# Optimization experiments

Hardware: AMD Instinct MI355X
Metric: run time of the kernel (lower is better)

## Reference

```python
import jax, jax.numpy as jnp
import numpy as np

B, Q, P, HID, H, KV, D = 2, 1024, 3072, 4096, 32, 8, 128
G = H // KV          # GQA group size
EPS = 1e-6
ROPE_THETA = 1e6


def setup_inputs() -> dict:
    key = jax.random.key(0)
    ks = jax.random.split(key, 8)
    hidden_states = jax.random.normal(ks[0], (B, Q, HID), jnp.float32)
    # real RoPE tables for positions [P, P+Q) (extend phase)
    pos = jnp.arange(P, P + Q, dtype=jnp.float32)
    inv_freq = 1.0 / (ROPE_THETA ** (jnp.arange(0, D, 2, dtype=jnp.float32) / D))
    freqs = pos[:, None] * inv_freq[None, :]            # [Q, D/2]
    emb = jnp.concatenate([freqs, freqs], axis=-1)       # [Q, D]
    cos = jnp.broadcast_to(jnp.cos(emb)[None], (B, Q, D)).astype(jnp.float32)
    sin = jnp.broadcast_to(jnp.sin(emb)[None], (B, Q, D)).astype(jnp.float32)
    k_cache = jax.random.normal(ks[1], (B, KV, P, D), jnp.float32)
    v_cache = jax.random.normal(ks[2], (B, KV, P, D), jnp.float32)
    s = 0.02
    Wq = jax.random.normal(ks[3], (HID, H * D), jnp.float32) * s
    Wk = jax.random.normal(ks[4], (HID, KV * D), jnp.float32) * s
    Wv = jax.random.normal(ks[5], (HID, KV * D), jnp.float32) * s
    Wo = jax.random.normal(ks[6], (H * D, HID), jnp.float32) * s
    q_norm_w = jnp.ones((D,), jnp.float32)
    k_norm_w = jnp.ones((D,), jnp.float32)
    return dict(hidden_states=hidden_states, cos=cos, sin=sin,
                k_cache=k_cache, v_cache=v_cache,
                Wq=Wq, Wk=Wk, Wv=Wv, Wo=Wo,
                q_norm_w=q_norm_w, k_norm_w=k_norm_w)


def _rmsnorm(x, w):
    var = jnp.mean(x * x, axis=-1, keepdims=True)
    return x * jax.lax.rsqrt(var + EPS) * w


def _rotate_half(x):
    x1, x2 = jnp.split(x, 2, axis=-1)
    return jnp.concatenate([-x2, x1], axis=-1)


def _rope(x, cos, sin):
    # x: [B, h, Q, D]; cos/sin: [B, Q, D] -> broadcast over heads
    c = cos[:, None, :, :]
    s = sin[:, None, :, :]
    return x * c + _rotate_half(x) * s


def reference(hidden_states, cos, sin, k_cache, v_cache,
              Wq, Wk, Wv, Wo, q_norm_w, k_norm_w):
    # projections
    q = (hidden_states @ Wq).reshape(B, Q, H, D)
    k = (hidden_states @ Wk).reshape(B, Q, KV, D)
    v = (hidden_states @ Wv).reshape(B, Q, KV, D)
    # per-head RMSNorm on q and k
    q = _rmsnorm(q, q_norm_w)
    k = _rmsnorm(k, k_norm_w)
    # [B, heads, Q, D]
    q = q.transpose(0, 2, 1, 3)
    k = k.transpose(0, 2, 1, 3)
    v = v.transpose(0, 2, 1, 3)
    q = _rope(q, cos, sin)
    k = _rope(k, cos, sin)
    # extend: concat cached prefix KV with new KV -> kv_len = P + Q
    K = jnp.concatenate([k_cache, k], axis=2)   # [B, KV, P+Q, D]
    V = jnp.concatenate([v_cache, v], axis=2)
    qg = q.reshape(B, KV, G, Q, D)
    scale = 1.0 / jnp.sqrt(jnp.float32(D))
    scores = jnp.einsum('bkgqd,bksd->bkgqs', qg, K) * scale  # [B,KV,G,Q,P+Q]
    # causal mask offset by prefix: query i sees keys <= P + i
    key_idx = jnp.arange(P + Q)
    mask = key_idx[None, :] <= (P + jnp.arange(Q))[:, None]  # [Q, P+Q]
    scores = jnp.where(mask[None, None, None], scores, jnp.float32(-1e30))
    attn = jax.nn.softmax(scores, axis=-1)
    out = jnp.einsum('bkgqs,bksd->bkgqd', attn, V)           # [B,KV,G,Q,D]
    out = out.reshape(B, H, Q, D).transpose(0, 2, 1, 3).reshape(B, Q, H * D)
    return out @ Wo
```

## Files before the change

kernel.cpp:

```cpp
#include <hip/hip_runtime.h>
#include <hip/hip_bf16.h>

#define B_ 2
#define Q_ 1024
#define P_ 3072
#define HID_ 4096
#define H_ 32
#define KV_ 8
#define D_ 128
#define S_ 4096
#define NQKV 6144
#define QSCALE 0.1275174432f

typedef __attribute__((ext_vector_type(4))) float f32x4;
typedef __attribute__((ext_vector_type(8))) unsigned short u16x8;
typedef __attribute__((ext_vector_type(4))) unsigned short u16x4;
typedef __attribute__((ext_vector_type(8))) __bf16 bf16x8;

__device__ __forceinline__ unsigned short f2bf(float f){
  unsigned u = __builtin_bit_cast(unsigned, f);
  unsigned r = (u + 0x7FFFu + ((u >> 16) & 1u)) >> 16;
  return (unsigned short)r;
}
__device__ __forceinline__ unsigned pk2bf(float lo, float hi){
  unsigned r;
  asm("v_cvt_pk_bf16_f32 %0, %1, %2" : "=v"(r) : "v"(lo), "v"(hi));
  return r;
}
__device__ __forceinline__ f32x4 mfma16(u16x8 a, u16x8 b, f32x4 c){
  return __builtin_amdgcn_mfma_f32_16x16x32_bf16(
      __builtin_bit_cast(bf16x8, a), __builtin_bit_cast(bf16x8, b), c, 0, 0, 0);
}
typedef const __attribute__((address_space(1))) void* gp1_t;
typedef __attribute__((address_space(3))) void* lp3_t;
__device__ __forceinline__ void gl16(const unsigned short* g, unsigned short* l){
  __builtin_amdgcn_global_load_lds((gp1_t)g, (lp3_t)l, 16, 0, 0);
}

#define N1_ 2097152
#define N2_ 1572864
__global__ __launch_bounds__(256) void prep(
    const float* __restrict__ hs, const float* __restrict__ kc,
    unsigned short* __restrict__ AH, unsigned short* __restrict__ Kb){
  const int PD = P_ * D_;
  const long SD = (long)S_ * D_;
  for(int i4 = blockIdx.x * 256 + threadIdx.x; i4 < N1_ + N2_; i4 += gridDim.x * 256){
    if(i4 < N1_){
      long i = (long)i4 * 4;
      float4 x = *(const float4*)(hs + i);
      *(u16x4*)(AH + i) = (u16x4){f2bf(x.x), f2bf(x.y), f2bf(x.z), f2bf(x.w)};
    } else {
      long i = (long)(i4 - N1_) * 4;
      int bkv = (int)(i / PD);
      int rem = (int)(i - (long)bkv * PD);
      long dst = (long)bkv * SD + rem;
      float4 k4 = *(const float4*)(kc + i);
      *(u16x4*)(Kb + dst) = (u16x4){f2bf(k4.x), f2bf(k4.y), f2bf(k4.z), f2bf(k4.w)};
    }
  }
}

__global__ __launch_bounds__(256) void convert_w(
    const float* __restrict__ Wq, const float* __restrict__ Wk,
    const float* __restrict__ Wv, const float* __restrict__ Wo,
    unsigned short* __restrict__ WT, unsigned short* __restrict__ WoT){
  __shared__ float tile[64][65];
  int x = blockIdx.x;
  const float* W; int ldn, n_off; unsigned short* dst; int n0;
  if(x < 64)      { W = Wq; ldn = 4096; n_off = 0;    dst = WT;  n0 = x * 64; }
  else if(x < 80) { W = Wk; ldn = 1024; n_off = 4096; dst = WT;  n0 = (x-64) * 64; }
  else if(x < 96) { W = Wv; ldn = 1024; n_off = 5120; dst = WT;  n0 = (x-80) * 64; }
  else            { W = Wo; ldn = 4096; n_off = 0;    dst = WoT; n0 = (x-96) * 64; }
  int k0 = blockIdx.y * 64;
  int tid = threadIdx.x;
  int r = tid >> 4, c = (tid & 15) * 4;
  #pragma unroll
  for(int j = 0; j < 4; ++j){
    float4 v = *(const float4*)(W + (long)(k0 + r + j*16) * ldn + n0 + c);
    tile[r + j*16][c] = v.x; tile[r + j*16][c+1] = v.y;
    tile[r + j*16][c+2] = v.z; tile[r + j*16][c+3] = v.w;
  }
  __syncthreads();
  #pragma unroll
  for(int j = 0; j < 4; ++j){
    int n = r + j*16;
    long o = (long)(n_off + n0 + n) * 4096 + k0 + c;
    *(u16x4*)(dst + o) = (u16x4){f2bf(tile[c][n]), f2bf(tile[c+1][n]),
                                 f2bf(tile[c+2][n]), f2bf(tile[c+3][n])};
  }
}

__global__ __launch_bounds__(256) void cache_vt(
    const float* __restrict__ vc, unsigned short* __restrict__ VT){
  __shared__ unsigned short T[128][72];
  int bkv = blockIdx.y;
  int s0 = blockIdx.x * 64;
  int tid = threadIdx.x;
  int r = tid >> 2, dblk = (tid & 3) * 32;
  const float* src = vc + ((long)bkv * P_ + s0 + r) * 128 + dblk;
  #pragma unroll
  for(int u = 0; u < 8; ++u){
    float4 v = *(const float4*)(src + u*4);
    T[dblk + u*4 + 0][r] = f2bf(v.x);
    T[dblk + u*4 + 1][r] = f2bf(v.y);
    T[dblk + u*4 + 2][r] = f2bf(v.z);
    T[dblk + u*4 + 3][r] = f2bf(v.w);
  }
  __syncthreads();
  int d = tid >> 1, sh = (tid & 1) * 32;
  unsigned short* dst = VT + ((long)bkv * 128 + d) * S_ + s0 + sh;
  #pragma unroll
  for(int u = 0; u < 4; ++u){
    u16x8 v;
    #pragma unroll
    for(int j = 0; j < 8; ++j) v[j] = T[d][sh + u*8 + j];
    *(u16x8*)(dst + u*8) = v;
  }
}

__global__ __launch_bounds__(128) void maxw(
    const float* __restrict__ qw, const float* __restrict__ kw, float* __restrict__ M){
  __shared__ float sa[2], sb[2];
  int t = threadIdx.x;
  float a = fabsf(qw[t]), b = fabsf(kw[t]);
  #pragma unroll
  for(int o = 32; o; o >>= 1){
    a = fmaxf(a, __shfl_xor(a, o));
    b = fmaxf(b, __shfl_xor(b, o));
  }
  if((t & 63) == 0){ sa[t >> 6] = a; sb[t >> 6] = b; }
  __syncthreads();
  if(t == 0){
    float mq = fmaxf(sa[0], sa[1]), mk = fmaxf(sb[0], sb[1]);
    M[0] = 128.0f * QSCALE * mq * mk * 1.01f + 0.25f;
  }
}

__global__ __launch_bounds__(256) void gemm_bf16(
    const unsigned short* __restrict__ Ag, const unsigned short* __restrict__ Bg,
    float* __restrict__ C, int nbx, int ldc){
  __shared__ __align__(16) unsigned short sA[4096], sB[4096];
  int tid = threadIdx.x;
  int nwg = nbx * 16;
  int lin = blockIdx.x;
  int cpx = nwg >> 3;
  int swz = (lin & 7) * cpx + (lin >> 3);
  int by = swz & 15, bx = swz >> 4;
  int m0 = by * 128, n0 = bx * 128;
  int lane = tid & 63, w = tid >> 6;
  int lr = lane & 15, lg = lane >> 4;
  int wm = (w >> 1) * 64, wn = (w & 1) * 64;
  int rowi = w * 16 + (lane >> 2);
  int cchunk = ((lane & 3) ^ ((lane >> 3) & 3)) << 3;
  const unsigned short* aP = Ag + (long)(m0 + rowi) * 4096 + cchunk;
  const unsigned short* bP = Bg + (long)(n0 + rowi) * 4096 + cchunk;
  const int step2 = 64 * 4096;
  unsigned short* dA = sA + w * 512;
  unsigned short* dB = sB + w * 512;
  int rdcol = (lg * 8) ^ (((lr >> 1) & 3) << 3);
  f32x4 zero = {0.f,0.f,0.f,0.f};
  f32x4 acc[4][4];
  #pragma unroll
  for(int mi=0;mi<4;++mi)
    #pragma unroll
    for(int ni=0;ni<4;++ni) acc[mi][ni] = zero;

  for(int kt = 0; kt < 128; ++kt){
    int kk = kt * 32;
    __syncthreads();
    gl16(aP + kk, dA);  gl16(aP + step2 + kk, dA + 2048);
    gl16(bP + kk, dB);  gl16(bP + step2 + kk, dB + 2048);
    __syncthreads();
    u16x8 ah[4];
    #pragma unroll
    for(int mi = 0; mi < 4; ++mi)
      ah[mi] = *(const u16x8*)(sA + (wm + mi*16 + lr) * 32 + rdcol);
    #pragma unroll
    for(int ni = 0; ni < 4; ++ni){
      u16x8 bh = *(const u16x8*)(sB + (wn + ni*16 + lr) * 32 + rdcol);
      #pragma unroll
      for(int mi = 0; mi < 4; ++mi)
        acc[mi][ni] = mfma16(ah[mi], bh, acc[mi][ni]);
    }
  }
  #pragma unroll
  for(int mi = 0; mi < 4; ++mi)
    #pragma unroll
    for(int r = 0; r < 4; ++r){
      long rowoff = (long)(m0 + wm + mi*16 + lg*4 + r) * ldc + n0 + wn + lr;
      #pragma unroll
      for(int ni = 0; ni < 4; ++ni)
        C[rowoff + ni*16] = acc[mi][ni][r];
    }
}

__global__ __launch_bounds__(256) void pp_qkv(
    const float* __restrict__ Craw, const float* __restrict__ cosb,
    const float* __restrict__ sinb, const float* __restrict__ qw,
    const float* __restrict__ kw, unsigned short* __restrict__ Qb,
    unsigned short* __restrict__ Kb, unsigned short* __restrict__ VT){
  int rid = blockIdx.x * 4 + (threadIdx.x >> 6);
  int lane = threadIdx.x & 63;
  if(rid < 65536){
    int b = rid >> 15;
    int rem = rid & 32767;
    int q = rem >> 5;
    int h = rem & 31;
    long rowoff = (long)(b * Q_ + q) * NQKV + h * 128;
    float x1 = Craw[rowoff + lane];
    float x2 = Craw[rowoff + 64 + lane];
    float ss = x1*x1 + x2*x2;
    for(int o = 32; o; o >>= 1) ss += __shfl_xor(ss, o);
    float norm = rsqrtf(ss * (1.0f/128.0f) + 1e-6f);
    float xn1 = x1 * norm * qw[lane];
    float xn2 = x2 * norm * qw[64 + lane];
    long co = (long)(b * Q_ + q) * 128;
    float c1 = cosb[co + lane],      s1 = sinb[co + lane];
    float c2 = cosb[co + 64 + lane], s2 = sinb[co + 64 + lane];
    float o1 = (xn1 * c1 - xn2 * s1) * QSCALE;
    float o2 = (xn2 * c2 + xn1 * s2) * QSCALE;
    long dst = ((long)(b * H_ + h) * Q_ + q) * 128;
    Qb[dst + lane] = f2bf(o1);
    Qb[dst + 64 + lane] = f2bf(o2);
  } else {
    int rid2 = rid - 65536;
    int b = rid2 >> 13;
    int rem = rid2 & 8191;
    int q = rem >> 3;
    int kv = rem & 7;
    int bkv = b * KV_ + kv;
    long rowoff = (long)(b * Q_ + q) * NQKV;
    float x1 = Craw[rowoff + 4096 + kv*128 + lane];
    float x2 = Craw[rowoff + 4096 + kv*128 + 64 + lane];
    float ss = x1*x1 + x2*x2;
    for(int o = 32; o; o >>= 1) ss += __shfl_xor(ss, o);
    float norm = rsqrtf(ss * (1.0f/128.0f) + 1e-6f);
    float xn1 = x1 * norm * kw[lane];
    float xn2 = x2 * norm * kw[64 + lane];
    long co = (long)(b * Q_ + q) * 128;
    float c1 = cosb[co + lane],      s1 = sinb[co + lane];
    float c2 = cosb[co + 64 + lane], s2 = sinb[co + 64 + lane];
    long dst = ((long)bkv * S_ + P_ + q) * 128;
    Kb[dst + lane]      = f2bf(xn1 * c1 - xn2 * s1);
    Kb[dst + 64 + lane] = f2bf(xn2 * c2 + xn1 * s2);
    float v1 = Craw[rowoff + 5120 + kv*128 + lane];
    float v2 = Craw[rowoff + 5120 + kv*128 + 64 + lane];
    VT[((long)bkv * 128 + lane) * S_ + P_ + q]      = f2bf(v1);
    VT[((long)bkv * 128 + 64 + lane) * S_ + P_ + q] = f2bf(v2);
  }
}

#define KVB 32
#define PSL 40
__global__ __launch_bounds__(256, 2) void attn(
    const unsigned short* __restrict__ Qg, const unsigned short* __restrict__ Kg,
    const unsigned short* __restrict__ VTg, const float* __restrict__ Mp,
    float* __restrict__ po, float* __restrict__ pl){
  __shared__ __align__(16) unsigned short Ks[2][KVB*128];
  __shared__ __align__(16) unsigned short Vs[2][128*KVB];
  __shared__ __align__(16) unsigned short Ps[4][64*PSL];
  int tid = threadIdx.x;
  int qb = blockIdx.x >> 1, sp = blockIdx.x & 1;
  int b = blockIdx.z, h = blockIdx.y, q0 = qb * 256;
  int kvh = h >> 2;
  int w = tid >> 6, lane = tid & 63, lr = lane & 15, lg = lane >> 4;
  int q0w = q0 + w * 64;
  float Mv = Mp[0];
  u16x8 qh[4][4];
  #pragma unroll
  for(int mi = 0; mi < 4; ++mi){
    long qbase = ((long)(b * H_ + h) * Q_ + q0w + mi*16 + lr) * 128;
    #pragma unroll
    for(int c = 0; c < 4; ++c)
      qh[mi][c] = *(const u16x8*)(Qg + qbase + c*32 + lg*8);
  }
  f32x4 minit = {-Mv, -Mv, -Mv, -Mv};
  f32x4 zero = {0.f,0.f,0.f,0.f};
  f32x4 o[4][8];
  #pragma unroll
  for(int mi = 0; mi < 4; ++mi)
    #pragma unroll
    for(int i = 0; i < 8; ++i) o[mi][i] = zero;
  float l[4] = {0.f, 0.f, 0.f, 0.f};
  long kb  = (long)(b * KV_ + kvh) * S_ * 128;
  long vb0 = (long)(b * KV_ + kvh) * 128 * (long)S_;
  int T = 104 + 8 * qb;
  int half = T >> 1;
  int t0 = sp ? half : 0;
  int t1 = sp ? T : half;
  int koff[2], voff[2], ldst[2];
  #pragma unroll
  for(int i = 0; i < 2; ++i){
    int L = (w*2 + i)*64 + lane;
    ldst[i] = L * 8;
    int r = L >> 4, c8 = (L & 15) ^ (r & 7);
    koff[i] = r*128 + c8*8;
    int d = L >> 2, sc = (L & 3) ^ (d & 3) ^ ((d >> 2) & 3);
    voff[i] = d*S_ + sc*8;
  }
  {
    const unsigned short* kg = Kg + kb + (long)t0 * (KVB*128);
    const unsigned short* vg = VTg + vb0 + t0 * KVB;
    #pragma unroll
    for(int i = 0; i < 2; ++i){
      gl16(kg + koff[i], &Ks[t0 & 1][ldst[i]]);
      gl16(vg + voff[i], &Vs[t0 & 1][ldst[i]]);
    }
  }
  __syncthreads();

  int lr7 = lr & 7;
  for(int t = t0; t < t1; ++t){
    int cur = t & 1;
    if(t + 1 < t1){
      int s1 = (t + 1) * KVB;
      const unsigned short* kg = Kg + kb + (long)s1 * 128;
      const unsigned short* vg = VTg + vb0 + s1;
      #pragma unroll
      for(int i = 0; i < 2; ++i){
        gl16(kg + koff[i], &Ks[cur^1][ldst[i]]);
        gl16(vg + voff[i], &Vs[cur^1][ldst[i]]);
      }
    }
    int s0 = t * KVB;
    if(s0 <= P_ + q0w + 63){
      f32x4 pacc[4][2];
      #pragma unroll
      for(int mi = 0; mi < 4; ++mi){ pacc[mi][0] = minit; pacc[mi][1] = minit; }
      __builtin_amdgcn_s_setprio(1);
      #pragma unroll
      for(int c = 0; c < 4; ++c)
        #pragma unroll
        for(int ni = 0; ni < 2; ++ni){
          u16x8 kh = *(const u16x8*)(&Ks[cur][(ni*16 + lr)*128 + (((c*4 + lg) ^ lr7) << 3)]);
          #pragma unroll
          for(int mi = 0; mi < 4; ++mi)
            pacc[mi][ni] = mfma16(kh, qh[mi][c], pacc[mi][ni]);
        }
      __builtin_amdgcn_s_setprio(0);
      if(s0 + KVB - 1 > P_ + q0w){
        #pragma unroll
        for(int mi = 0; mi < 4; ++mi){
          int qrow = q0w + mi*16 + lr;
          #pragma unroll
          for(int ni = 0; ni < 2; ++ni)
            #pragma unroll
            for(int r = 0; r < 4; ++r){
              int skey = s0 + ni*16 + lg*4 + r;
              if(skey > P_ + qrow) pacc[mi][ni][r] = -1e30f;
            }
        }
      }
      #pragma unroll
      for(int mi = 0; mi < 4; ++mi){
        float rs = 0.f;
        #pragma unroll
        for(int ni = 0; ni < 2; ++ni){
          float p0 = exp2f(pacc[mi][ni][0]);
          float p1 = exp2f(pacc[mi][ni][1]);
          float p2 = exp2f(pacc[mi][ni][2]);
          float p3 = exp2f(pacc[mi][ni][3]);
          rs += (p0 + p1) + (p2 + p3);
          uint2 pw; pw.x = pk2bf(p0, p1); pw.y = pk2bf(p2, p3);
          *(uint2*)(&Ps[w][(mi*16 + lr)*PSL + ni*16 + lg*4]) = pw;
        }
        l[mi] += rs;
      }
      u16x8 pa[4];
      #pragma unroll
      for(int mi = 0; mi < 4; ++mi)
        pa[mi] = *(const u16x8*)(&Ps[w][(mi*16 + lr)*PSL + lg*8]);
      __builtin_amdgcn_s_setprio(1);
      #pragma unroll
      for(int ni = 0; ni < 8; ++ni){
        int d = ni*16 + lr;
        int scs = lg ^ (lr & 3) ^ ((lr >> 2) & 3);
        u16x8 vbf = *(const u16x8*)(&Vs[cur][d*32 + (scs << 3)]);
        #pragma unroll
        for(int mi = 0; mi < 4; ++mi)
          o[mi][ni] = mfma16(pa[mi], vbf, o[mi][ni]);
      }
      __builtin_amdgcn_s_setprio(0);
    }
    __syncthreads();
  }
  int bh = b * H_ + h;
  #pragma unroll
  for(int mi = 0; mi < 4; ++mi){
    float lt = l[mi];
    lt += __shfl_xor(lt, 16);
    lt += __shfl_xor(lt, 32);
    #pragma unroll
    for(int r = 0; r < 4; ++r){
      int qrow = q0w + mi*16 + lg*4 + r;
      long obase = ((long)(sp*64 + bh) * Q_ + qrow) * 128;
      #pragma unroll
      for(int ni = 0; ni < 8; ++ni)
        po[obase + ni*16 + lr] = o[mi][ni][r];
    }
    if(lane < 16)
      pl[(sp*64 + bh) * Q_ + q0w + mi*16 + lane] = lt;
  }
}

__global__ __launch_bounds__(256) void combine(
    const float* __restrict__ po, const float* __restrict__ pl,
    unsigned short* __restrict__ OH){
  int idx = blockIdx.x * 256 + threadIdx.x;
  int row = idx >> 5;
  int d4 = (idx & 31) * 4;
  int bh = row >> 10, q = row & 1023;
  int b = bh >> 5, h = bh & 31;
  float lsum = pl[bh*1024 + q] + pl[65536 + bh*1024 + q];
  float inv = 1.0f / lsum;
  float4 a = *(const float4*)(po + (long)row*128 + d4);
  float4 c = *(const float4*)(po + 8388608L + (long)row*128 + d4);
  u16x4 r = { f2bf((a.x + c.x) * inv), f2bf((a.y + c.y) * inv),
              f2bf((a.z + c.z) * inv), f2bf((a.w + c.w) * inv) };
  *(u16x4*)(OH + ((long)(b*1024 + q))*4096 + h*128 + d4) = r;
}

extern "C" void kernel_launch(void* const* d_in, const int* in_sizes, int n_in,
                              void* d_out, int out_size, void* d_ws, size_t ws_size,
                              hipStream_t stream){
  const float* hs   = (const float*)d_in[0];
  const float* cosb = (const float*)d_in[1];
  const float* sinb = (const float*)d_in[2];
  const float* kc   = (const float*)d_in[3];
  const float* vc   = (const float*)d_in[4];
  const float* Wq   = (const float*)d_in[5];
  const float* Wk   = (const float*)d_in[6];
  const float* Wv   = (const float*)d_in[7];
  const float* Wo   = (const float*)d_in[8];
  const float* qw   = (const float*)d_in[9];
  const float* kw   = (const float*)d_in[10];
  char* ws = (char*)d_ws;
  float* Craw          = (float*)ws;
  unsigned short* OH   = (unsigned short*)ws;
  unsigned short* WT   = (unsigned short*)(ws + 50331648);
  float* PO            = (float*)(ws + 50331648);
  unsigned short* WoT  = (unsigned short*)(ws + 117440512);
  unsigned short* AH   = (unsigned short*)(ws + 150994944);
  unsigned short* QB   = (unsigned short*)(ws + 150994944);
  unsigned short* KB   = (unsigned short*)(ws + 167772160);
  unsigned short* VT   = (unsigned short*)(ws + 184549376);
  float* PL            = (float*)(ws + 201326592);
  float* MW            = (float*)(ws + 201981952);
  float* Out = (float*)d_out;

  prep<<<dim3(2048), dim3(256), 0, stream>>>(hs, kc, AH, KB);
  convert_w<<<dim3(160, 64), dim3(256), 0, stream>>>(Wq, Wk, Wv, Wo, WT, WoT);
  cache_vt<<<dim3(48, 16), dim3(256), 0, stream>>>(vc, VT);
  maxw<<<dim3(1), dim3(128), 0, stream>>>(qw, kw, MW);
  gemm_bf16<<<dim3(768), dim3(256), 0, stream>>>(AH, WT, Craw, 48, NQKV);
  pp_qkv<<<dim3(20480), dim3(256), 0, stream>>>(Craw, cosb, sinb, qw, kw, QB, KB, VT);
  attn<<<dim3(8, 32, 2), dim3(256), 0, stream>>>(QB, KB, VT, MW, PO, PL);
  combine<<<dim3(8192), dim3(256), 0, stream>>>(PO, PL, OH);
  gemm_bf16<<<dim3(512), dim3(256), 0, stream>>>(OH, WoT, Out, 32, 4096);
}
```

Before: 516.8 us.

## Drop split-KV attention and fuse normalization into attention epilogue

```diff
diff --git a/kernel.cpp b/kernel.cpp
--- a/kernel.cpp
+++ b/kernel.cpp
@@ -26,6 +26,13 @@
   unsigned r;
   asm("v_cvt_pk_bf16_f32 %0, %1, %2" : "=v"(r) : "v"(lo), "v"(hi));
   return r;
+}
+__device__ __forceinline__ float fexp2(float x){
+#if __has_builtin(__builtin_amdgcn_exp2f)
+  return __builtin_amdgcn_exp2f(x);
+#else
+  float r; asm("v_exp_f32 %0, %1" : "=v"(r) : "v"(x)); return r;
+#endif
 }
 __device__ __forceinline__ f32x4 mfma16(u16x8 a, u16x8 b, f32x4 c){
   return __builtin_amdgcn_mfma_f32_16x16x32_bf16(
@@ -255,12 +262,12 @@
 __global__ __launch_bounds__(256, 2) void attn(
     const unsigned short* __restrict__ Qg, const unsigned short* __restrict__ Kg,
     const unsigned short* __restrict__ VTg, const float* __restrict__ Mp,
-    float* __restrict__ po, float* __restrict__ pl){
+    unsigned short* __restrict__ Og){
   __shared__ __align__(16) unsigned short Ks[2][KVB*128];
   __shared__ __align__(16) unsigned short Vs[2][128*KVB];
   __shared__ __align__(16) unsigned short Ps[4][64*PSL];
   int tid = threadIdx.x;
-  int qb = blockIdx.x >> 1, sp = blockIdx.x & 1;
+  int qb = blockIdx.x;
   int b = blockIdx.z, h = blockIdx.y, q0 = qb * 256;
   int kvh = h >> 2;
   int w = tid >> 6, lane = tid & 63, lr = lane & 15, lg = lane >> 4;
@@ -285,9 +292,6 @@
   long kb  = (long)(b * KV_ + kvh) * S_ * 128;
   long vb0 = (long)(b * KV_ + kvh) * 128 * (long)S_;
   int T = 104 + 8 * qb;
-  int half = T >> 1;
-  int t0 = sp ? half : 0;
-  int t1 = sp ? T : half;
   int koff[2], voff[2], ldst[2];
   #pragma unroll
   for(int i = 0; i < 2; ++i){
@@ -295,24 +299,27 @@
     ldst[i] = L * 8;
     int r = L >> 4, c8 = (L & 15) ^ (r & 7);
     koff[i] = r*128 + c8*8;
-    int d = L >> 2, sc = (L & 3) ^ (d & 3) ^ ((d >> 2) & 3);
-    voff[i] = d*S_ + sc*8;
+    int d = ((L >> 3) << 1) | (L & 1);
+    int sm = (L >> 1) & 3;
+    int g = (d & 3) ^ ((d >> 2) & 3);
+    voff[i] = d * S_ + ((sm ^ g) << 3);
   }
   {
-    const unsigned short* kg = Kg + kb + (long)t0 * (KVB*128);
-    const unsigned short* vg = VTg + vb0 + t0 * KVB;
+    const unsigned short* kg = Kg + kb;
+    const unsigned short* vg = VTg + vb0;
     #pragma unroll
     for(int i = 0; i < 2; ++i){
-      gl16(kg + koff[i], &Ks[t0 & 1][ldst[i]]);
-      gl16(vg + voff[i], &Vs[t0 & 1][ldst[i]]);
+      gl16(kg + koff[i], &Ks[0][ldst[i]]);
+      gl16(vg + voff[i], &Vs[0][ldst[i]]);
     }
   }
   __syncthreads();
 
   int lr7 = lr & 7;
-  for(int t = t0; t < t1; ++t){
+  int gread = (lr & 3) ^ ((lr >> 2) & 3);
+  for(int t = 0; t < T; ++t){
     int cur = t & 1;
-    if(t + 1 < t1){
+    if(t + 1 < T){
       int s1 = (t + 1) * KVB;
       const unsigned short* kg = Kg + kb + (long)s1 * 128;
       const unsigned short* vg = VTg + vb0 + s1;
@@ -356,10 +363,10 @@
         float rs = 0.f;
         #pragma unroll
         for(int ni = 0; ni < 2; ++ni){
-          float p0 = exp2f(pacc[mi][ni][0]);
-          float p1 = exp2f(pacc[mi][ni][1]);
-          float p2 = exp2f(pacc[mi][ni][2]);
-          float p3 = exp2f(pacc[mi][ni][3]);
+          float p0 = fexp2(pacc[mi][ni][0]);
+          float p1 = fexp2(pacc[mi][ni][1]);
+          float p2 = fexp2(pacc[mi][ni][2]);
+          float p3 = fexp2(pacc[mi][ni][3]);
           rs += (p0 + p1) + (p2 + p3);
           uint2 pw; pw.x = pk2bf(p0, p1); pw.y = pk2bf(p2, p3);
           *(uint2*)(&Ps[w][(mi*16 + lr)*PSL + ni*16 + lg*4]) = pw;
@@ -374,8 +381,8 @@
       #pragma unroll
       for(int ni = 0; ni < 8; ++ni){
         int d = ni*16 + lr;
-        int scs = lg ^ (lr & 3) ^ ((lr >> 2) & 3);
-        u16x8 vbf = *(const u16x8*)(&Vs[cur][d*32 + (scs << 3)]);
+        int voffr = ((d >> 1) << 6) + ((lg ^ gread) << 4) + ((d & 1) << 3);
+        u16x8 vbf = *(const u16x8*)(&Vs[cur][voffr]);
         #pragma unroll
         for(int mi = 0; mi < 4; ++mi)
           o[mi][ni] = mfma16(pa[mi], vbf, o[mi][ni]);
@@ -384,40 +391,22 @@
     }
     __syncthreads();
   }
-  int bh = b * H_ + h;
   #pragma unroll
   for(int mi = 0; mi < 4; ++mi){
     float lt = l[mi];
     lt += __shfl_xor(lt, 16);
     lt += __shfl_xor(lt, 32);
+    float linv = 1.0f / lt;
     #pragma unroll
     for(int r = 0; r < 4; ++r){
+      float li = __shfl(linv, (lg << 4) | (lg*4 + r));
       int qrow = q0w + mi*16 + lg*4 + r;
-      long obase = ((long)(sp*64 + bh) * Q_ + qrow) * 128;
+      long obase = (long)(b * Q_ + qrow) * 4096 + h * 128;
       #pragma unroll
       for(int ni = 0; ni < 8; ++ni)
-        po[obase + ni*16 + lr] = o[mi][ni][r];
-    }
-    if(lane < 16)
-      pl[(sp*64 + bh) * Q_ + q0w + mi*16 + lane] = lt;
-  }
-}
-
-__global__ __launch_bounds__(256) void combine(
-    const float* __restrict__ po, const float* __restrict__ pl,
-    unsigned short* __restrict__ OH){
-  int idx = blockIdx.x * 256 + threadIdx.x;
-  int row = idx >> 5;
-  int d4 = (idx & 31) * 4;
-  int bh = row >> 10, q = row & 1023;
-  int b = bh >> 5, h = bh & 31;
-  float lsum = pl[bh*1024 + q] + pl[65536 + bh*1024 + q];
-  float inv = 1.0f / lsum;
-  float4 a = *(const float4*)(po + (long)row*128 + d4);
-  float4 c = *(const float4*)(po + 8388608L + (long)row*128 + d4);
-  u16x4 r = { f2bf((a.x + c.x) * inv), f2bf((a.y + c.y) * inv),
-              f2bf((a.z + c.z) * inv), f2bf((a.w + c.w) * inv) };
-  *(u16x4*)(OH + ((long)(b*1024 + q))*4096 + h*128 + d4) = r;
+        Og[obase + ni*16 + lr] = f2bf(o[mi][ni][r] * li);
+    }
+  }
 }
 
 extern "C" void kernel_launch(void* const* d_in, const int* in_sizes, int n_in,
@@ -438,13 +427,11 @@
   float* Craw          = (float*)ws;
   unsigned short* OH   = (unsigned short*)ws;
   unsigned short* WT   = (unsigned short*)(ws + 50331648);
-  float* PO            = (float*)(ws + 50331648);
   unsigned short* WoT  = (unsigned short*)(ws + 117440512);
   unsigned short* AH   = (unsigned short*)(ws + 150994944);
   unsigned short* QB   = (unsigned short*)(ws + 150994944);
   unsigned short* KB   = (unsigned short*)(ws + 167772160);
   unsigned short* VT   = (unsigned short*)(ws + 184549376);
-  float* PL            = (float*)(ws + 201326592);
   float* MW            = (float*)(ws + 201981952);
   float* Out = (float*)d_out;
 
@@ -454,7 +441,6 @@
   maxw<<<dim3(1), dim3(128), 0, stream>>>(qw, kw, MW);
   gemm_bf16<<<dim3(768), dim3(256), 0, stream>>>(AH, WT, Craw, 48, NQKV);
   pp_qkv<<<dim3(20480), dim3(256), 0, stream>>>(Craw, cosb, sinb, qw, kw, QB, KB, VT);
-  attn<<<dim3(8, 32, 2), dim3(256), 0, stream>>>(QB, KB, VT, MW, PO, PL);
-  combine<<<dim3(8192), dim3(256), 0, stream>>>(PO, PL, OH);
+  attn<<<dim3(4, 32, 2), dim3(256), 0, stream>>>(QB, KB, VT, MW, OH);
   gemm_bf16<<<dim3(512), dim3(256), 0, stream>>>(OH, WoT, Out, 32, 4096);
 }
```

New measurement: 600.4 us. 16.2% more time.
